# Optimization experiments

Measured on AMD Instinct MI355X. Metric: run time of the kernel, lower is better.

Reference implementation:

```python
import jax, jax.numpy as jnp
import numpy as np

D, C, H, W = 8, 512, 64, 64


def setup_inputs() -> dict:
    key = jax.random.key(0)
    k1, k2, k3 = jax.random.split(key, 3)
    x = jax.random.normal(k1, (D, C, H, W), dtype=jnp.float32)
    atten = jax.random.normal(k2, (D, C, C), dtype=jnp.float32)
    gamma = jax.random.normal(k3, (1,), dtype=jnp.float32)
    return {"x": x, "atten": atten, "gamma": gamma}


def reference(x, atten, gamma):
    d, c, h, w = x.shape
    q = x.reshape(d, c, h * w)              # q == v == flattened x; k = q^T
    # energy[d, i, j] = <channel_i, channel_j> over spatial positions
    energy = jnp.einsum('din,djn->dij', q, q)
    # max-centering: rowmax - energy (note the sign flip vs standard softmax)
    energy_new = jnp.max(energy, axis=-1, keepdims=True) - energy
    attention = jax.nn.softmax(energy_new, axis=-1)
    attention = jax.nn.softmax(attention + atten, axis=-1)
    # out = attention^T @ v : out[d, j, n] = sum_i attention[d, i, j] * v[d, i, n]
    out = jnp.einsum('dij,din->djn', attention, q).reshape(d, c, h, w)
    return gamma * out + x
```

## Files before the change

kernel.cpp:

```cpp
#include <hip/hip_runtime.h>
#include <hip/hip_bf16.h>

#define DD 8
#define CC 512
#define NN 4096

typedef __bf16 bf16x8 __attribute__((ext_vector_type(8)));
typedef float  f32x4  __attribute__((ext_vector_type(4)));
typedef ushort ush8   __attribute__((ext_vector_type(8)));

__device__ __forceinline__ ushort f2bf(float f) {
  unsigned u = __float_as_uint(f);
  u = (u + 0x7fffu + ((u >> 16) & 1u)) >> 16;
  return (ushort)u;
}
__device__ __forceinline__ float bf2f(ushort h) {
  return __uint_as_float(((unsigned)h) << 16);
}

__device__ __forceinline__ void gl_lds16(const ushort* g, ushort* l) {
  __builtin_amdgcn_global_load_lds(
      (const __attribute__((address_space(1))) void*)g,
      (__attribute__((address_space(3))) void*)l, 16, 0, 0);
}

__global__ __launch_bounds__(256) void k0_convert(
    const float* __restrict__ x, ushort* __restrict__ qh,
    ushort* __restrict__ ql, ushort* __restrict__ qt) {
  int d = blockIdx.z, ct = blockIdx.y, nt = blockIdx.x;
  __shared__ ushort T[64][64];
  int t = threadIdx.x;
  int rr = t >> 3;
  int j  = t & 7;
  int n8 = j * 8;
  const float* xb = x + ((size_t)(d * CC + ct * 64)) * NN + nt * 64;
#pragma unroll
  for (int it = 0; it < 2; ++it) {
    int r = it * 32 + rr;
    const float* xr = xb + (size_t)r * NN + n8;
    float4 v0 = *(const float4*)xr;
    float4 v1 = *(const float4*)(xr + 4);
    float vv[8] = {v0.x, v0.y, v0.z, v0.w, v1.x, v1.y, v1.z, v1.w};
    ush8 h, l;
#pragma unroll
    for (int k = 0; k < 8; ++k) {
      ushort hh = f2bf(vv[k]);
      h[k] = hh;
      l[k] = f2bf(vv[k] - bf2f(hh));
    }
    size_t qi = ((size_t)(d * CC + ct * 64 + r)) * NN + nt * 64 + n8;
    *(ush8*)(qh + qi) = h;
    *(ush8*)(ql + qi) = l;
    *(ush8*)&T[r][(j ^ (r >> 3)) * 8] = h;
  }
  __syncthreads();
#pragma unroll
  for (int it = 0; it < 2; ++it) {
    int n = it * 32 + rr;
    int c8 = n8;
    ush8 o;
#pragma unroll
    for (int cc = 0; cc < 8; ++cc) {
      int c = c8 + cc;
      int chunk = (n >> 3) ^ (c >> 3);
      o[cc] = T[c][chunk * 8 + (n & 7)];
    }
    *(ush8*)&qt[((size_t)(d * NN + nt * 64 + n)) * CC + ct * 64 + c8] = o;
  }
}

__global__ __launch_bounds__(256, 2) void k1_gram(
    const ushort* __restrict__ qh, const ushort* __restrict__ ql,
    float* __restrict__ Ep, int ns, int nkk, int ksp) {
  __shared__ ushort As[2][128 * 32];
  __shared__ ushort Bs[2][128 * 32];
  int b = blockIdx.x;
  int s = b % ns;
  int rem = b / ns;
  int tile = rem % 10, d = rem / 10;
  int tm = (int)((0x3221110000ULL >> (tile * 4)) & 15ULL);
  int tn = (int)((0x3323213210ULL >> (tile * 4)) & 15ULL);
  int t = threadIdx.x, lane = t & 63, w = t >> 6;
  int wm = (w >> 1) * 64, wn = (w & 1) * 64;
  int qd = lane >> 4, fr = lane & 15;

  const ushort* srcbase = (w & 1) ? ql : qh;
  int rowblk = (w < 2) ? tm : tn;
  const ushort* gsrc = srcbase +
      ((size_t)(d * CC + rowblk * 128 + (lane >> 2))) * NN +
      (size_t)s * ksp + (lane & 3) * 8;
  ushort* ldst = (w < 2) ? As[w & 1] : Bs[w & 1];

  f32x4 acc[4][4];
#pragma unroll
  for (int i = 0; i < 4; ++i)
#pragma unroll
    for (int j = 0; j < 4; ++j) acc[i][j] = (f32x4){0.f, 0.f, 0.f, 0.f};

  for (int kk = 0; kk < nkk; ++kk) {
    __syncthreads();
    const ushort* g0 = gsrc + (size_t)kk * 32;
#pragma unroll
    for (int c = 0; c < 8; ++c)
      gl_lds16(g0 + (size_t)c * 16 * NN, ldst + c * 512);
    __syncthreads();

    bf16x8 ah[4], al[4];
#pragma unroll
    for (int mi = 0; mi < 4; ++mi) {
      int off = (wm + mi * 16 + fr) * 32 + qd * 8;
      ah[mi] = *(const bf16x8*)&As[0][off];
      al[mi] = *(const bf16x8*)&As[1][off];
    }
#pragma unroll
    for (int ni = 0; ni < 4; ++ni) {
      int off = (wn + ni * 16 + fr) * 32 + qd * 8;
      bf16x8 bh = *(const bf16x8*)&Bs[0][off];
      bf16x8 bl = *(const bf16x8*)&Bs[1][off];
#pragma unroll
      for (int mi = 0; mi < 4; ++mi) {
        acc[mi][ni] = __builtin_amdgcn_mfma_f32_16x16x32_bf16(ah[mi], bh, acc[mi][ni], 0, 0, 0);
        acc[mi][ni] = __builtin_amdgcn_mfma_f32_16x16x32_bf16(ah[mi], bl, acc[mi][ni], 0, 0, 0);
        acc[mi][ni] = __builtin_amdgcn_mfma_f32_16x16x32_bf16(al[mi], bh, acc[mi][ni], 0, 0, 0);
      }
    }
  }

  size_t ebase = ((size_t)(s * DD + d)) * ((size_t)CC * CC);
#pragma unroll
  for (int mi = 0; mi < 4; ++mi) {
    int r0 = tm * 128 + wm + mi * 16 + qd * 4;
#pragma unroll
    for (int ni = 0; ni < 4; ++ni) {
      int c0 = tn * 128 + wn + ni * 16 + fr;
      float* ep = Ep + ebase + (size_t)r0 * CC + c0;
#pragma unroll
      for (int r = 0; r < 4; ++r) ep[(size_t)r * CC] = acc[mi][ni][r];
    }
  }
  if (tm != tn) {
#pragma unroll
    for (int mi = 0; mi < 4; ++mi) {
      int r0 = tm * 128 + wm + mi * 16 + qd * 4;
#pragma unroll
      for (int ni = 0; ni < 4; ++ni) {
        int c0 = tn * 128 + wn + ni * 16 + fr;
        float4 v = make_float4(acc[mi][ni][0], acc[mi][ni][1],
                               acc[mi][ni][2], acc[mi][ni][3]);
        *(float4*)(Ep + ebase + (size_t)c0 * CC + r0) = v;
      }
    }
  }
}

__device__ __forceinline__ float wmin(float v) {
#pragma unroll
  for (int o = 32; o > 0; o >>= 1) v = fminf(v, __shfl_xor(v, o));
  return v;
}
__device__ __forceinline__ float wmax(float v) {
#pragma unroll
  for (int o = 32; o > 0; o >>= 1) v = fmaxf(v, __shfl_xor(v, o));
  return v;
}
__device__ __forceinline__ float wsum(float v) {
#pragma unroll
  for (int o = 32; o > 0; o >>= 1) v += __shfl_xor(v, o);
  return v;
}

__global__ __launch_bounds__(256) void k2_softmax(
    const float* __restrict__ Ep, const float* __restrict__ atten,
    ushort* __restrict__ a2t, int ns) {
  int d = blockIdx.y, i0 = blockIdx.x * 8;
  int t = threadIdx.x, lane = t & 63, w = t >> 6;
  int j8 = lane * 8;
  __shared__ ushort T[8][520];
  const size_t SP = (size_t)DD * CC * CC;

#pragma unroll
  for (int r2 = 0; r2 < 2; ++r2) {
    int ri = w * 2 + r2;
    size_t base = ((size_t)(d * CC + i0 + ri)) * CC + j8;
    f32x4 a0 = (f32x4){0.f, 0.f, 0.f, 0.f};
    f32x4 a1 = (f32x4){0.f, 0.f, 0.f, 0.f};
    for (int s = 0; s < ns; ++s) {
      const float* p = Ep + (size_t)s * SP + base;
      a0 += *(const f32x4*)p;
      a1 += *(const f32x4*)(p + 4);
    }
    float mn = fminf(fminf(fminf(a0[0], a0[1]), fminf(a0[2], a0[3])),
                     fminf(fminf(a1[0], a1[1]), fminf(a1[2], a1[3])));
    mn = wmin(mn);
    float p0 = __expf(mn - a0[0]), p1 = __expf(mn - a0[1]);
    float p2 = __expf(mn - a0[2]), p3 = __expf(mn - a0[3]);
    float p4 = __expf(mn - a1[0]), p5 = __expf(mn - a1[1]);
    float p6 = __expf(mn - a1[2]), p7 = __expf(mn - a1[3]);
    float s1 = wsum(p0 + p1 + p2 + p3 + p4 + p5 + p6 + p7);
    float inv1 = 1.0f / s1;
    const float* ap = atten + base;
    f32x4 t0 = *(const f32x4*)ap;
    f32x4 t1 = *(const f32x4*)(ap + 4);
    float u0 = p0 * inv1 + t0[0], u1 = p1 * inv1 + t0[1];
    float u2 = p2 * inv1 + t0[2], u3 = p3 * inv1 + t0[3];
    float u4 = p4 * inv1 + t1[0], u5 = p5 * inv1 + t1[1];
    float u6 = p6 * inv1 + t1[2], u7 = p7 * inv1 + t1[3];
    float mx = wmax(fmaxf(fmaxf(fmaxf(u0, u1), fmaxf(u2, u3)),
                          fmaxf(fmaxf(u4, u5), fmaxf(u6, u7))));
    float q0 = __expf(u0 - mx), q1 = __expf(u1 - mx);
    float q2 = __expf(u2 - mx), q3 = __expf(u3 - mx);
    float q4 = __expf(u4 - mx), q5 = __expf(u5 - mx);
    float q6 = __expf(u6 - mx), q7 = __expf(u7 - mx);
    float s2 = wsum(q0 + q1 + q2 + q3 + q4 + q5 + q6 + q7);
    float inv2 = 1.0f / s2;
    ush8 o;
    o[0] = f2bf(q0 * inv2); o[1] = f2bf(q1 * inv2);
    o[2] = f2bf(q2 * inv2); o[3] = f2bf(q3 * inv2);
    o[4] = f2bf(q4 * inv2); o[5] = f2bf(q5 * inv2);
    o[6] = f2bf(q6 * inv2); o[7] = f2bf(q7 * inv2);
    *(ush8*)&T[ri][j8] = o;
  }
  __syncthreads();
#pragma unroll
  for (int it = 0; it < 2; ++it) {
    int j = t + it * 256;
    ush8 o;
#pragma unroll
    for (int k = 0; k < 8; ++k) o[k] = T[k][j];
    *(ush8*)&a2t[((size_t)(d * CC + j)) * CC + i0] = o;
  }
}

__global__ __launch_bounds__(256, 4) void k3_out(
    const ushort* __restrict__ a2t, const ushort* __restrict__ qt,
    const float* __restrict__ x, const float* __restrict__ gamma,
    float* __restrict__ out) {
  __shared__ ushort As[128 * 64];
  __shared__ ushort Bs[128 * 64];
  int b = blockIdx.x;
  int nt = b & 31, jt = (b >> 5) & 3, d = b >> 7;
  int t = threadIdx.x, lane = t & 63, w = t >> 6;
  int wj = (w >> 1) * 64, wn2 = (w & 1) * 64;
  int qd = lane >> 4, fr = lane & 15;

  const ushort* src = (w < 2)
      ? (a2t + (size_t)d * CC * CC + (size_t)(jt * 128) * CC)
      : (qt + (size_t)d * NN * CC + (size_t)(nt * 128) * CC);
  ushort* ldst = (w < 2) ? As : Bs;
  int wbase = (w & 1) * 64;
  const ushort* g0 = src + ((size_t)(wbase + (lane >> 3))) * CC + (lane & 7) * 8;
  ushort* l0 = ldst + wbase * 64;

  f32x4 acc[4][4];
#pragma unroll
  for (int i = 0; i < 4; ++i)
#pragma unroll
    for (int j = 0; j < 4; ++j) acc[i][j] = (f32x4){0.f, 0.f, 0.f, 0.f};

  for (int kk = 0; kk < CC / 64; ++kk) {
    __syncthreads();
#pragma unroll
    for (int c = 0; c < 8; ++c)
      gl_lds16(g0 + kk * 64 + (size_t)(c * 8) * CC, l0 + c * 512);
    __syncthreads();

#pragma unroll
    for (int h = 0; h < 2; ++h) {
      bf16x8 qf[4];
#pragma unroll
      for (int ii = 0; ii < 4; ++ii)
        qf[ii] = *(const bf16x8*)&Bs[(wn2 + ii * 16 + fr) * 64 + h * 32 + qd * 8];
#pragma unroll
      for (int jj = 0; jj < 4; ++jj) {
        bf16x8 af = *(const bf16x8*)&As[(wj + jj * 16 + fr) * 64 + h * 32 + qd * 8];
#pragma unroll
        for (int ii = 0; ii < 4; ++ii)
          acc[ii][jj] = __builtin_amdgcn_mfma_f32_16x16x32_bf16(qf[ii], af, acc[ii][jj], 0, 0, 0);
      }
    }
  }

  float g = gamma[0];
#pragma unroll
  for (int ii = 0; ii < 4; ++ii) {
    int n0 = nt * 128 + wn2 + ii * 16 + qd * 4;
#pragma unroll
    for (int jj = 0; jj < 4; ++jj) {
      int j = jt * 128 + wj + jj * 16 + fr;
      size_t idx = ((size_t)(d * CC + j)) * NN + n0;
      float4 xv = *(const float4*)(x + idx);
      float4 ov = make_float4(g * acc[ii][jj][0] + xv.x,
                              g * acc[ii][jj][1] + xv.y,
                              g * acc[ii][jj][2] + xv.z,
                              g * acc[ii][jj][3] + xv.w);
      *(float4*)(out + idx) = ov;
    }
  }
}

extern "C" void kernel_launch(void* const* d_in, const int* in_sizes, int n_in,
                              void* d_out, int out_size, void* d_ws, size_t ws_size,
                              hipStream_t stream) {
  (void)in_sizes; (void)n_in; (void)out_size;
  const float* x     = (const float*)d_in[0];
  const float* atten = (const float*)d_in[1];
  const float* gamma = (const float*)d_in[2];
  float* out = (float*)d_out;

  char* ws = (char*)d_ws;
  ushort* qh  = (ushort*)(ws);
  ushort* ql  = (ushort*)(ws + 33554432);
  ushort* qt  = (ushort*)(ws + 67108864);
  ushort* a2t = (ushort*)(ws + 100663296);
  float*  Ep  = (float*) (ws + 104857600);

  int ns = (ws_size >= 104857600ULL + 8ULL * 8388608ULL) ? 8 : 4;
  int ksp = NN / ns;
  int nkk = ksp / 32;

  k0_convert<<<dim3(64, 8, 8), 256, 0, stream>>>(x, qh, ql, qt);
  k1_gram   <<<dim3(80 * ns), 256, 0, stream>>>(qh, ql, Ep, ns, nkk, ksp);
  k2_softmax<<<dim3(64, 8), 256, 0, stream>>>(Ep, atten, a2t, ns);
  k3_out    <<<dim3(1024), 256, 0, stream>>>(a2t, qt, x, gamma, out);
}
```

Baseline: 248.7 us.

## Shrink k3_out tiles to 128x64 with 32-wide K steps for more blocks

The output GEMM kernel moves from 128x128 output tiles with 64-wide K slices to 128x64 tiles with 32-wide K slices. Each wave now computes a 32x64 sub-tile, and the block count doubles to 2048. The smaller LDS footprint and accumulator set, together with a launch bound of 6, aim to raise occupancy and spread the work more evenly across CUs. In exchange, the A tile is reloaded twice as often, each block does less MFMA work per barrier, and the number of sync points per block doubles.

Result: faster. 235.8 us (-5.2%).

```diff
diff --git a/kernel.cpp b/kernel.cpp
--- a/kernel.cpp
+++ b/kernel.cpp
@@ -231,68 +231,70 @@
   }
 }
 
-__global__ __launch_bounds__(256, 4) void k3_out(
+__global__ __launch_bounds__(256, 6) void k3_out(
     const ushort* __restrict__ a2t, const ushort* __restrict__ qt,
     const float* __restrict__ x, const float* __restrict__ gamma,
     float* __restrict__ out) {
-  __shared__ ushort As[128 * 64];
-  __shared__ ushort Bs[128 * 64];
+  __shared__ ushort As[128 * 32];
+  __shared__ ushort Bs[64 * 32];
   int b = blockIdx.x;
-  int nt = b & 31, jt = (b >> 5) & 3, d = b >> 7;
+  int nt = b & 63, jt = (b >> 6) & 3, d = b >> 8;
   int t = threadIdx.x, lane = t & 63, w = t >> 6;
-  int wj = (w >> 1) * 64, wn2 = (w & 1) * 64;
+  int wj = w * 32;
   int qd = lane >> 4, fr = lane & 15;
 
-  const ushort* src = (w < 2)
-      ? (a2t + (size_t)d * CC * CC + (size_t)(jt * 128) * CC)
-      : (qt + (size_t)d * NN * CC + (size_t)(nt * 128) * CC);
-  ushort* ldst = (w < 2) ? As : Bs;
-  int wbase = (w & 1) * 64;
-  const ushort* g0 = src + ((size_t)(wbase + (lane >> 3))) * CC + (lane & 7) * 8;
-  ushort* l0 = ldst + wbase * 64;
-
-  f32x4 acc[4][4];
+  const ushort* src;
+  ushort* l0;
+  int nchunk;
+  if (w < 2) {
+    src = a2t + (size_t)d * CC * CC + (size_t)(jt * 128 + w * 64) * CC;
+    l0 = As + w * 64 * 32;
+    nchunk = 4;
+  } else {
+    src = qt + (size_t)d * NN * CC + (size_t)(nt * 64 + (w - 2) * 32) * CC;
+    l0 = Bs + (w - 2) * 32 * 32;
+    nchunk = 2;
+  }
+  const ushort* g0 = src + (size_t)(lane >> 2) * CC + (lane & 3) * 8;
+
+  f32x4 acc[4][2];
 #pragma unroll
   for (int i = 0; i < 4; ++i)
 #pragma unroll
-    for (int j = 0; j < 4; ++j) acc[i][j] = (f32x4){0.f, 0.f, 0.f, 0.f};
-
-  for (int kk = 0; kk < CC / 64; ++kk) {
+    for (int j = 0; j < 2; ++j) acc[i][j] = (f32x4){0.f, 0.f, 0.f, 0.f};
+
+  for (int kk = 0; kk < CC / 32; ++kk) {
     __syncthreads();
-#pragma unroll
-    for (int c = 0; c < 8; ++c)
-      gl_lds16(g0 + kk * 64 + (size_t)(c * 8) * CC, l0 + c * 512);
+    for (int c = 0; c < nchunk; ++c)
+      gl_lds16(g0 + kk * 32 + (size_t)(c * 16) * CC, l0 + c * 512);
     __syncthreads();
 
-#pragma unroll
-    for (int h = 0; h < 2; ++h) {
-      bf16x8 qf[4];
-#pragma unroll
-      for (int ii = 0; ii < 4; ++ii)
-        qf[ii] = *(const bf16x8*)&Bs[(wn2 + ii * 16 + fr) * 64 + h * 32 + qd * 8];
-#pragma unroll
-      for (int jj = 0; jj < 4; ++jj) {
-        bf16x8 af = *(const bf16x8*)&As[(wj + jj * 16 + fr) * 64 + h * 32 + qd * 8];
-#pragma unroll
-        for (int ii = 0; ii < 4; ++ii)
-          acc[ii][jj] = __builtin_amdgcn_mfma_f32_16x16x32_bf16(qf[ii], af, acc[ii][jj], 0, 0, 0);
-      }
+    bf16x8 qf[4];
+#pragma unroll
+    for (int ni = 0; ni < 4; ++ni)
+      qf[ni] = *(const bf16x8*)&Bs[(ni * 16 + fr) * 32 + qd * 8];
+#pragma unroll
+    for (int ji = 0; ji < 2; ++ji) {
+      bf16x8 af = *(const bf16x8*)&As[(wj + ji * 16 + fr) * 32 + qd * 8];
+#pragma unroll
+      for (int ni = 0; ni < 4; ++ni)
+        acc[ni][ji] = __builtin_amdgcn_mfma_f32_16x16x32_bf16(qf[ni], af, acc[ni][ji], 0, 0, 0);
     }
   }
 
   float g = gamma[0];
 #pragma unroll
-  for (int ii = 0; ii < 4; ++ii) {
-    int n0 = nt * 128 + wn2 + ii * 16 + qd * 4;
-#pragma unroll
-    for (int jj = 0; jj < 4; ++jj) {
-      int j = jt * 128 + wj + jj * 16 + fr;
+  for (int ni = 0; ni < 4; ++ni) {
+    int n0 = nt * 64 + ni * 16 + qd * 4;
+#pragma unroll
+    for (int ji = 0; ji < 2; ++ji) {
+      int j = jt * 128 + wj + ji * 16 + fr;
       size_t idx = ((size_t)(d * CC + j)) * NN + n0;
       float4 xv = *(const float4*)(x + idx);
-      float4 ov = make_float4(g * acc[ii][jj][0] + xv.x,
-                              g * acc[ii][jj][1] + xv.y,
-                              g * acc[ii][jj][2] + xv.z,
-                              g * acc[ii][jj][3] + xv.w);
+      float4 ov = make_float4(g * acc[ni][ji][0] + xv.x,
+                              g * acc[ni][ji][1] + xv.y,
+                              g * acc[ni][ji][2] + xv.z,
+                              g * acc[ni][ji][3] + xv.w);
       *(float4*)(out + idx) = ov;
     }
   }
@@ -321,5 +323,5 @@
   k0_convert<<<dim3(64, 8, 8), 256, 0, stream>>>(x, qh, ql, qt);
   k1_gram   <<<dim3(80 * ns), 256, 0, stream>>>(qh, ql, Ep, ns, nkk, ksp);
   k2_softmax<<<dim3(64, 8), 256, 0, stream>>>(Ep, atten, a2t, ns);
-  k3_out    <<<dim3(1024), 256, 0, stream>>>(a2t, qt, x, gamma, out);
-}
+  k3_out    <<<dim3(2048), 256, 0, stream>>>(a2t, qt, x, gamma, out);
+}
```
